# Kernel tuning notes

Hardware: AMD Instinct MI355X
Metric: run time of the kernel (lower is better)

## Reference

```python
import jax, jax.numpy as jnp
import numpy as np

B, N, M, H = 32, 1024, 256, 128


def setup_inputs() -> dict:
    key = jax.random.key(0)
    kA, kh, kW1, kW2 = jax.random.split(key, 4)
    A = jax.random.uniform(kA, (B, N, N), dtype=jnp.float32)
    h = jax.random.normal(kh, (B, N, M), dtype=jnp.float32)
    # torch Linear default init scale ~ 1/sqrt(fan_in)
    W1 = jax.random.normal(kW1, (M, H), dtype=jnp.float32) / np.sqrt(M)
    b1 = jnp.zeros((H,), dtype=jnp.float32)
    W2 = jax.random.normal(kW2, (H, M), dtype=jnp.float32) / np.sqrt(H)
    b2 = jnp.zeros((M,), dtype=jnp.float32)
    return {"A": A, "h": h, "W1": W1, "b1": b1, "W2": W2, "b2": b2}


def reference(A, h, W1, b1, W2, b2):
    # k = bmm(A, h) / 3 : [B,N,M]
    k = jnp.einsum('bij,bjm->bim', A, h) / 3.0
    # eta_g: Linear -> ReLU -> Linear
    k = jax.nn.relu(k @ W1 + b1) @ W2 + b2
    # A_mask = max over last dim of A, keepdims -> [B,N,1]
    A_mask = jnp.max(A, axis=-1, keepdims=True)
    # gated combine: k*mask + h*(mask-1)*(-1) == k*mask + h*(1-mask)
    return k * A_mask + h * (1.0 - A_mask)
```

## Files before the change

kernel.cpp:

```cpp
#include <hip/hip_runtime.h>

typedef __attribute__((ext_vector_type(8))) short bf16x8;
typedef __attribute__((ext_vector_type(4))) float f32x4;
typedef __attribute__((ext_vector_type(8))) unsigned short u16x8;

#define BB 32
#define NN 1024
#define MM 256
#define HH 128

__device__ __forceinline__ unsigned short f2bf(float f) {
  union { float f; unsigned int u; } c; c.f = f;
  unsigned int u = c.u + 0x7fffu + ((c.u >> 16) & 1u);
  return (unsigned short)(u >> 16);
}
__device__ __forceinline__ unsigned int pack2(float lo, float hi) {
  return (unsigned int)f2bf(lo) | ((unsigned int)f2bf(hi) << 16);
}

__global__ __launch_bounds__(256)
void k_transpose_h(const float* __restrict__ hg, unsigned short* __restrict__ hTg) {
  __shared__ unsigned short tile[64][65];
  int bid = blockIdx.x;
  int b = bid >> 6;
  int t = bid & 63;
  int k0 = (t >> 2) << 6;
  int m0 = (t & 3) << 6;
  int tt = threadIdx.x;
  {
    int r = tt >> 2;
    int cg = (tt & 3) << 4;
    const float* src = hg + (((size_t)b * NN + k0 + r) * MM + m0 + cg);
#pragma unroll
    for (int i = 0; i < 4; ++i) {
      float4 v = reinterpret_cast<const float4*>(src)[i];
      tile[r][cg + i * 4 + 0] = f2bf(v.x);
      tile[r][cg + i * 4 + 1] = f2bf(v.y);
      tile[r][cg + i * 4 + 2] = f2bf(v.z);
      tile[r][cg + i * 4 + 3] = f2bf(v.w);
    }
  }
  __syncthreads();
  {
    int mr = tt >> 2;
    int kc = (tt & 3) << 4;
    alignas(16) unsigned short tmp[16];
#pragma unroll
    for (int i = 0; i < 16; ++i) tmp[i] = tile[kc + i][mr];
    unsigned short* dst = hTg + (((size_t)b * MM + m0 + mr) * NN + k0 + kc);
    *reinterpret_cast<u16x8*>(dst)     = *reinterpret_cast<u16x8*>(tmp);
    *reinterpret_cast<u16x8*>(dst + 8) = *reinterpret_cast<u16x8*>(tmp + 8);
  }
}

__global__ __launch_bounds__(256)
void k_transpose_w(const float* __restrict__ W1, const float* __restrict__ W2,
                   unsigned short* __restrict__ W1T, unsigned short* __restrict__ W2T) {
  int idx = blockIdx.x * 256 + threadIdx.x;
  if (idx < MM * HH) {
    int hc = idx >> 8;
    int m  = idx & 255;
    W1T[idx] = f2bf(W1[m * HH + hc]);
  } else {
    int j = idx - MM * HH;
    int m  = j >> 7;
    int hd = j & 127;
    W2T[j] = f2bf(W2[hd * MM + m]);
  }
}

__global__ __launch_bounds__(512, 1)
void k_fused(const float* __restrict__ Ag, const float* __restrict__ hg,
             const unsigned short* __restrict__ hTg,
             const unsigned short* __restrict__ W1Tg,
             const unsigned short* __restrict__ W2Tg,
             const float* __restrict__ b1g, const float* __restrict__ b2g,
             float* __restrict__ outg) {
  __shared__ __align__(16) char smem[131072];
  __shared__ float smax[128];

  const int tid  = threadIdx.x;
  const int lane = tid & 63;
  const int wid  = tid >> 6;
  const int wr   = wid >> 2;
  const int wc   = wid & 3;
  const int l15  = lane & 15;
  const int lg   = lane >> 4;

  const int bid = blockIdx.x;
  const int b   = bid >> 3;
  const int r0  = (bid & 7) << 7;

  const float* Ab = Ag + ((size_t)b * NN + r0) * NN;
  const unsigned short* hTb = hTg + (size_t)b * MM * NN;

  f32x4 acc[4][4];
#pragma unroll
  for (int m = 0; m < 4; ++m)
#pragma unroll
    for (int n = 0; n < 4; ++n) acc[m][n] = f32x4{0.f, 0.f, 0.f, 0.f};

  float pmax = -1e30f;
  const int arow = tid >> 2;
  const int acg  = (tid & 3) << 4;

  for (int k0 = 0; k0 < NN; k0 += 64) {
    {
      const float* src = Ab + (size_t)arow * NN + k0 + acg;
      float4 v0 = reinterpret_cast<const float4*>(src)[0];
      float4 v1 = reinterpret_cast<const float4*>(src)[1];
      float4 v2 = reinterpret_cast<const float4*>(src)[2];
      float4 v3 = reinterpret_cast<const float4*>(src)[3];
      float m0 = fmaxf(fmaxf(v0.x, v0.y), fmaxf(v0.z, v0.w));
      float m1 = fmaxf(fmaxf(v1.x, v1.y), fmaxf(v1.z, v1.w));
      float m2 = fmaxf(fmaxf(v2.x, v2.y), fmaxf(v2.z, v2.w));
      float m3 = fmaxf(fmaxf(v3.x, v3.y), fmaxf(v3.z, v3.w));
      pmax = fmaxf(pmax, fmaxf(fmaxf(m0, m1), fmaxf(m2, m3)));
      unsigned int p0 = pack2(v0.x, v0.y), p1 = pack2(v0.z, v0.w);
      unsigned int p2 = pack2(v1.x, v1.y), p3 = pack2(v1.z, v1.w);
      unsigned int p4 = pack2(v2.x, v2.y), p5 = pack2(v2.z, v2.w);
      unsigned int p6 = pack2(v3.x, v3.y), p7 = pack2(v3.z, v3.w);
      int base = arow * 128;
      int sw   = (arow & 7) << 4;
      *reinterpret_cast<uint4*>(smem + base + ((acg * 2) ^ sw))      = make_uint4(p0, p1, p2, p3);
      *reinterpret_cast<uint4*>(smem + base + ((acg * 2 + 16) ^ sw)) = make_uint4(p4, p5, p6, p7);
    }
    {
      const int hc = (tid & 7) << 3;
#pragma unroll
      for (int i = 0; i < 4; ++i) {
        int hrow = (i << 6) + (tid >> 3);
        uint4 v = *reinterpret_cast<const uint4*>(hTb + (size_t)hrow * NN + k0 + hc);
        *reinterpret_cast<uint4*>(smem + 16384 + hrow * 128 + ((hc * 2) ^ ((hrow & 7) << 4))) = v;
      }
    }
    __syncthreads();
#pragma unroll
    for (int kk = 0; kk < 2; ++kk) {
      const int kb = (kk * 32 + (lg << 3)) * 2;
      bf16x8 af[4], bfr[4];
#pragma unroll
      for (int m = 0; m < 4; ++m) {
        int row = (wr << 6) + (m << 4) + l15;
        af[m] = *reinterpret_cast<const bf16x8*>(smem + row * 128 + (kb ^ ((row & 7) << 4)));
      }
#pragma unroll
      for (int n = 0; n < 4; ++n) {
        int col = (wc << 6) + (n << 4) + l15;
        bfr[n] = *reinterpret_cast<const bf16x8*>(smem + 16384 + col * 128 + (kb ^ ((col & 7) << 4)));
      }
#pragma unroll
      for (int m = 0; m < 4; ++m)
#pragma unroll
        for (int n = 0; n < 4; ++n)
          acc[m][n] = __builtin_amdgcn_mfma_f32_16x16x32_bf16(af[m], bfr[n], acc[m][n], 0, 0, 0);
    }
    __syncthreads();
  }

  {
    float v = pmax;
    v = fmaxf(v, __shfl_xor(v, 1));
    v = fmaxf(v, __shfl_xor(v, 2));
    if ((tid & 3) == 0) smax[arow] = v;
  }

  {
    const float inv3 = 1.0f / 3.0f;
#pragma unroll
    for (int m = 0; m < 4; ++m)
#pragma unroll
      for (int n = 0; n < 4; ++n) {
        int col = (wc << 6) + (n << 4) + l15;
#pragma unroll
        for (int j = 0; j < 4; ++j) {
          int row = (wr << 6) + (m << 4) + (lg << 2) + j;
          *reinterpret_cast<unsigned short*>(smem + row * 512 + ((col * 2) ^ ((row & 7) << 4))) =
              f2bf(acc[m][n][j] * inv3);
        }
      }
  }
  {
#pragma unroll
    for (int i = 0; i < 8; ++i) {
      int c = (i << 9) + tid;
      int row = c >> 5;
      int bc  = (c & 31) << 4;
      uint4 v = *reinterpret_cast<const uint4*>(W1Tg + ((size_t)c << 3));
      *reinterpret_cast<uint4*>(smem + 65536 + row * 512 + (bc ^ ((row & 7) << 4))) = v;
    }
  }
  __syncthreads();

  f32x4 acc1[4][2];
#pragma unroll
  for (int m = 0; m < 4; ++m)
#pragma unroll
    for (int n = 0; n < 2; ++n) acc1[m][n] = f32x4{0.f, 0.f, 0.f, 0.f};
#pragma unroll
  for (int kk = 0; kk < 8; ++kk) {
    const int kb = (kk * 32 + (lg << 3)) * 2;
    bf16x8 af[4], bfr[2];
#pragma unroll
    for (int m = 0; m < 4; ++m) {
      int row = (wr << 6) + (m << 4) + l15;
      af[m] = *reinterpret_cast<const bf16x8*>(smem + row * 512 + (kb ^ ((row & 7) << 4)));
    }
#pragma unroll
    for (int n = 0; n < 2; ++n) {
      int col = (wc << 5) + (n << 4) + l15;
      bfr[n] = *reinterpret_cast<const bf16x8*>(smem + 65536 + col * 512 + (kb ^ ((col & 7) << 4)));
    }
#pragma unroll
    for (int m = 0; m < 4; ++m)
#pragma unroll
      for (int n = 0; n < 2; ++n)
        acc1[m][n] = __builtin_amdgcn_mfma_f32_16x16x32_bf16(af[m], bfr[n], acc1[m][n], 0, 0, 0);
  }
  __syncthreads();

  {
#pragma unroll
    for (int n = 0; n < 2; ++n) {
      int col = (wc << 5) + (n << 4) + l15;
      float bias = b1g[col];
#pragma unroll
      for (int m = 0; m < 4; ++m)
#pragma unroll
        for (int j = 0; j < 4; ++j) {
          int row = (wr << 6) + (m << 4) + (lg << 2) + j;
          float v = fmaxf(acc1[m][n][j] + bias, 0.f);
          *reinterpret_cast<unsigned short*>(smem + row * 256 + ((col * 2) ^ ((row & 7) << 4))) = f2bf(v);
        }
    }
  }
  {
#pragma unroll
    for (int i = 0; i < 8; ++i) {
      int c = (i << 9) + tid;
      int row = c >> 4;
      int bc  = (c & 15) << 4;
      uint4 v = *reinterpret_cast<const uint4*>(W2Tg + ((size_t)c << 3));
      *reinterpret_cast<uint4*>(smem + 65536 + row * 256 + (bc ^ ((row & 7) << 4))) = v;
    }
  }
  __syncthreads();

  f32x4 acc2[4][4];
#pragma unroll
  for (int m = 0; m < 4; ++m)
#pragma unroll
    for (int n = 0; n < 4; ++n) acc2[m][n] = f32x4{0.f, 0.f, 0.f, 0.f};
#pragma unroll
  for (int kk = 0; kk < 4; ++kk) {
    const int kb = (kk * 32 + (lg << 3)) * 2;
    bf16x8 af[4], bfr[4];
#pragma unroll
    for (int m = 0; m < 4; ++m) {
      int row = (wr << 6) + (m << 4) + l15;
      af[m] = *reinterpret_cast<const bf16x8*>(smem + row * 256 + (kb ^ ((row & 7) << 4)));
    }
#pragma unroll
    for (int n = 0; n < 4; ++n) {
      int col = (wc << 6) + (n << 4) + l15;
      bfr[n] = *reinterpret_cast<const bf16x8*>(smem + 65536 + col * 256 + (kb ^ ((col & 7) << 4)));
    }
#pragma unroll
    for (int m = 0; m < 4; ++m)
#pragma unroll
      for (int n = 0; n < 4; ++n)
        acc2[m][n] = __builtin_amdgcn_mfma_f32_16x16x32_bf16(af[m], bfr[n], acc2[m][n], 0, 0, 0);
  }

  {
#pragma unroll
    for (int n = 0; n < 4; ++n) {
      int col = (wc << 6) + (n << 4) + l15;
      float b2v = b2g[col];
#pragma unroll
      for (int m = 0; m < 4; ++m)
#pragma unroll
        for (int j = 0; j < 4; ++j) {
          int row = (wr << 6) + (m << 4) + (lg << 2) + j;
          float kv = acc2[m][n][j] + b2v;
          float mask = smax[row];
          size_t gidx = ((size_t)b * NN + r0 + row) * MM + col;
          float hv = hg[gidx];
          outg[gidx] = kv * mask + hv * (1.f - mask);
        }
    }
  }
}

extern "C" void kernel_launch(void* const* d_in, const int* in_sizes, int n_in,
                              void* d_out, int out_size, void* d_ws, size_t ws_size,
                              hipStream_t stream) {
  (void)in_sizes; (void)n_in; (void)out_size; (void)ws_size;
  const float* A  = (const float*)d_in[0];
  const float* h  = (const float*)d_in[1];
  const float* W1 = (const float*)d_in[2];
  const float* b1 = (const float*)d_in[3];
  const float* W2 = (const float*)d_in[4];
  const float* b2 = (const float*)d_in[5];
  float* out = (float*)d_out;

  unsigned short* hT  = (unsigned short*)d_ws;
  unsigned short* W1T = (unsigned short*)((char*)d_ws + (size_t)BB * MM * NN * 2);
  unsigned short* W2T = W1T + MM * HH;

  k_transpose_h<<<BB * 64, 256, 0, stream>>>(h, hT);
  k_transpose_w<<<256, 256, 0, stream>>>(W1, W2, W1T, W2T);
  k_fused<<<BB * 8, 512, 0, stream>>>(A, h, hT, W1T, W2T, b1, b2, out);
}
```

Measured before the change: 71.80 us.

## Double-buffer A/h tiles in LDS with register prefetch, remap blocks across batches

The main loop becomes a two-stage software pipeline. Global loads for the next 64-wide K slice of A and hT are issued into registers before the current slice is converted and written to one of two LDS buffers. This leaves one barrier per slice instead of two, and global-load latency overlaps with MFMA work. Block indexing is also changed so consecutive blocks cover different batches instead of consecutive row tiles of the same batch. The cost is extra VGPRs for the in-flight prefetch registers and twice the LDS staging space.

```diff
diff --git a/kernel.cpp b/kernel.cpp
--- a/kernel.cpp
+++ b/kernel.cpp
@@ -69,6 +69,48 @@
   }
 }
 
+#define A0_OFF 0
+#define A1_OFF 16384
+#define H0_OFF 32768
+#define H1_OFF 65536
+
+__device__ __forceinline__ void issueA(const float* src, float4 r[4]) {
+#pragma unroll
+  for (int i = 0; i < 4; ++i) r[i] = reinterpret_cast<const float4*>(src)[i];
+}
+__device__ __forceinline__ void issueH(const unsigned short* src, uint4 r[4]) {
+#pragma unroll
+  for (int i = 0; i < 4; ++i) r[i] = *reinterpret_cast<const uint4*>(src + (size_t)i * 64 * NN);
+}
+__device__ __forceinline__ float cvtWriteA(char* smem, int arow, int acg, const float4 r[4]) {
+  float m0 = fmaxf(fmaxf(r[0].x, r[0].y), fmaxf(r[0].z, r[0].w));
+  float m1 = fmaxf(fmaxf(r[1].x, r[1].y), fmaxf(r[1].z, r[1].w));
+  float m2 = fmaxf(fmaxf(r[2].x, r[2].y), fmaxf(r[2].z, r[2].w));
+  float m3 = fmaxf(fmaxf(r[3].x, r[3].y), fmaxf(r[3].z, r[3].w));
+  unsigned int p0 = pack2(r[0].x, r[0].y), p1 = pack2(r[0].z, r[0].w);
+  unsigned int p2 = pack2(r[1].x, r[1].y), p3 = pack2(r[1].z, r[1].w);
+  unsigned int p4 = pack2(r[2].x, r[2].y), p5 = pack2(r[2].z, r[2].w);
+  unsigned int p6 = pack2(r[3].x, r[3].y), p7 = pack2(r[3].z, r[3].w);
+  int base = arow * 128;
+  int sw   = (arow & 7) << 4;
+  *reinterpret_cast<uint4*>(smem + base + ((acg * 2) ^ sw))      = make_uint4(p0, p1, p2, p3);
+  *reinterpret_cast<uint4*>(smem + base + ((acg * 2 + 16) ^ sw)) = make_uint4(p4, p5, p6, p7);
+  return fmaxf(fmaxf(m0, m1), fmaxf(m2, m3));
+}
+__device__ __forceinline__ void writeH(char* smem, int tid, const uint4 r[4]) {
+  const int hc = (tid & 7) << 3;
+#pragma unroll
+  for (int i = 0; i < 4; ++i) {
+    int hrow = (i << 6) + (tid >> 3);
+    *reinterpret_cast<uint4*>(smem + hrow * 128 + ((hc * 2) ^ ((hrow & 7) << 4))) = r[i];
+  }
+}
+
+#define PIPE_BARRIER() do { \
+  asm volatile("s_waitcnt lgkmcnt(0)" ::: "memory"); \
+  __builtin_amdgcn_s_barrier(); \
+  asm volatile("" ::: "memory"); } while (0)
+
 __global__ __launch_bounds__(512, 1)
 void k_fused(const float* __restrict__ Ag, const float* __restrict__ hg,
              const unsigned short* __restrict__ hTg,
@@ -88,8 +130,8 @@
   const int lg   = lane >> 4;
 
   const int bid = blockIdx.x;
-  const int b   = bid >> 3;
-  const int r0  = (bid & 7) << 7;
+  const int b   = bid & 31;
+  const int r0  = (bid >> 5) << 7;
 
   const float* Ab = Ag + ((size_t)b * NN + r0) * NN;
   const unsigned short* hTb = hTg + (size_t)b * MM * NN;
@@ -103,60 +145,59 @@
   float pmax = -1e30f;
   const int arow = tid >> 2;
   const int acg  = (tid & 3) << 4;
-
-  for (int k0 = 0; k0 < NN; k0 += 64) {
-    {
-      const float* src = Ab + (size_t)arow * NN + k0 + acg;
-      float4 v0 = reinterpret_cast<const float4*>(src)[0];
-      float4 v1 = reinterpret_cast<const float4*>(src)[1];
-      float4 v2 = reinterpret_cast<const float4*>(src)[2];
-      float4 v3 = reinterpret_cast<const float4*>(src)[3];
-      float m0 = fmaxf(fmaxf(v0.x, v0.y), fmaxf(v0.z, v0.w));
-      float m1 = fmaxf(fmaxf(v1.x, v1.y), fmaxf(v1.z, v1.w));
-      float m2 = fmaxf(fmaxf(v2.x, v2.y), fmaxf(v2.z, v2.w));
-      float m3 = fmaxf(fmaxf(v3.x, v3.y), fmaxf(v3.z, v3.w));
-      pmax = fmaxf(pmax, fmaxf(fmaxf(m0, m1), fmaxf(m2, m3)));
-      unsigned int p0 = pack2(v0.x, v0.y), p1 = pack2(v0.z, v0.w);
-      unsigned int p2 = pack2(v1.x, v1.y), p3 = pack2(v1.z, v1.w);
-      unsigned int p4 = pack2(v2.x, v2.y), p5 = pack2(v2.z, v2.w);
-      unsigned int p6 = pack2(v3.x, v3.y), p7 = pack2(v3.z, v3.w);
-      int base = arow * 128;
-      int sw   = (arow & 7) << 4;
-      *reinterpret_cast<uint4*>(smem + base + ((acg * 2) ^ sw))      = make_uint4(p0, p1, p2, p3);
-      *reinterpret_cast<uint4*>(smem + base + ((acg * 2 + 16) ^ sw)) = make_uint4(p4, p5, p6, p7);
-    }
-    {
-      const int hc = (tid & 7) << 3;
-#pragma unroll
-      for (int i = 0; i < 4; ++i) {
-        int hrow = (i << 6) + (tid >> 3);
-        uint4 v = *reinterpret_cast<const uint4*>(hTb + (size_t)hrow * NN + k0 + hc);
-        *reinterpret_cast<uint4*>(smem + 16384 + hrow * 128 + ((hc * 2) ^ ((hrow & 7) << 4))) = v;
-      }
-    }
-    __syncthreads();
-#pragma unroll
-    for (int kk = 0; kk < 2; ++kk) {
-      const int kb = (kk * 32 + (lg << 3)) * 2;
-      bf16x8 af[4], bfr[4];
-#pragma unroll
-      for (int m = 0; m < 4; ++m) {
-        int row = (wr << 6) + (m << 4) + l15;
-        af[m] = *reinterpret_cast<const bf16x8*>(smem + row * 128 + (kb ^ ((row & 7) << 4)));
-      }
-#pragma unroll
-      for (int n = 0; n < 4; ++n) {
-        int col = (wc << 6) + (n << 4) + l15;
-        bfr[n] = *reinterpret_cast<const bf16x8*>(smem + 16384 + col * 128 + (kb ^ ((col & 7) << 4)));
-      }
-#pragma unroll
-      for (int m = 0; m < 4; ++m)
-#pragma unroll
-        for (int n = 0; n < 4; ++n)
-          acc[m][n] = __builtin_amdgcn_mfma_f32_16x16x32_bf16(af[m], bfr[n], acc[m][n], 0, 0, 0);
-    }
-    __syncthreads();
-  }
+  const float* Asrc = Ab + (size_t)arow * NN + acg;
+  const unsigned short* Hsrc = hTb + (size_t)(tid >> 3) * NN + ((tid & 7) << 3);
+
+  float4 a0[4], a1[4];
+  uint4  h0[4], h1[4];
+
+#define CONSUME(AOFF, HOFF)                                                          \
+  do {                                                                               \
+    _Pragma("unroll")                                                                \
+    for (int kk = 0; kk < 2; ++kk) {                                                 \
+      const int kb = (kk * 32 + (lg << 3)) * 2;                                      \
+      bf16x8 af[4], bfr[4];                                                          \
+      _Pragma("unroll")                                                              \
+      for (int m = 0; m < 4; ++m) {                                                  \
+        int row = (wr << 6) + (m << 4) + l15;                                        \
+        af[m] = *reinterpret_cast<const bf16x8*>(smem + (AOFF) + row * 128 +         \
+                                                 (kb ^ ((row & 7) << 4)));           \
+      }                                                                              \
+      _Pragma("unroll")                                                              \
+      for (int n = 0; n < 4; ++n) {                                                  \
+        int col = (wc << 6) + (n << 4) + l15;                                        \
+        bfr[n] = *reinterpret_cast<const bf16x8*>(smem + (HOFF) + col * 128 +        \
+                                                  (kb ^ ((col & 7) << 4)));          \
+      }                                                                              \
+      _Pragma("unroll")                                                              \
+      for (int m = 0; m < 4; ++m)                                                    \
+        _Pragma("unroll")                                                            \
+        for (int n = 0; n < 4; ++n)                                                  \
+          acc[m][n] = __builtin_amdgcn_mfma_f32_16x16x32_bf16(af[m], bfr[n],         \
+                                                              acc[m][n], 0, 0, 0);   \
+    }                                                                                \
+  } while (0)
+
+  issueA(Asrc, a0);
+  issueH(Hsrc, h0);
+  for (int t2 = 0; t2 < 8; ++t2) {
+    const int k0 = t2 << 7;
+    issueA(Asrc + k0 + 64, a1);
+    issueH(Hsrc + k0 + 64, h1);
+    pmax = fmaxf(pmax, cvtWriteA(smem + A0_OFF, arow, acg, a0));
+    writeH(smem + H0_OFF, tid, h0);
+    PIPE_BARRIER();
+    CONSUME(A0_OFF, H0_OFF);
+    if (t2 != 7) {
+      issueA(Asrc + k0 + 128, a0);
+      issueH(Hsrc + k0 + 128, h0);
+    }
+    pmax = fmaxf(pmax, cvtWriteA(smem + A1_OFF, arow, acg, a1));
+    writeH(smem + H1_OFF, tid, h1);
+    PIPE_BARRIER();
+    CONSUME(A1_OFF, H1_OFF);
+  }
+  __syncthreads();
 
   {
     float v = pmax;
@@ -290,6 +331,7 @@
         }
     }
   }
+#undef CONSUME
 }
 
 extern "C" void kernel_launch(void* const* d_in, const int* in_sizes, int n_in,
```

After: 75.98 us. 5.8% more time.

## Retile fused kernel to 32-row blocks with register-prefetched A/h pipeline

Applied to the files above, without the earlier changes.

Shrinks each block from 128 rows/512 threads to 32 rows/256 threads, launching 1024 blocks with about 24KB of LDS so several blocks can fit per CU. The A tile is prefetched four stages ahead into registers and double-buffered in LDS, while h fragments are loaded straight from global memory into registers instead of going through LDS. W1/W2 fragments are also read directly from global memory. The aim is to hide global-load latency and raise occupancy on a bandwidth-bound kernel, at the cost of more register pressure and h being re-read by four times as many blocks.

```diff
diff --git a/kernel.cpp b/kernel.cpp
--- a/kernel.cpp
+++ b/kernel.cpp
@@ -69,219 +69,227 @@
   }
 }
 
-__global__ __launch_bounds__(512, 1)
+#define ABUF(i) ((i) * 4096)
+#define KLD 8192
+#define CLD 0
+
+#define PIPE_BARRIER() do { \
+  asm volatile("s_waitcnt lgkmcnt(0)" ::: "memory"); \
+  __builtin_amdgcn_s_barrier(); } while (0)
+
+__global__ __launch_bounds__(256, 3)
 void k_fused(const float* __restrict__ Ag, const float* __restrict__ hg,
              const unsigned short* __restrict__ hTg,
              const unsigned short* __restrict__ W1Tg,
              const unsigned short* __restrict__ W2Tg,
              const float* __restrict__ b1g, const float* __restrict__ b2g,
              float* __restrict__ outg) {
-  __shared__ __align__(16) char smem[131072];
-  __shared__ float smax[128];
+  __shared__ __align__(16) char smem[24576];
+  __shared__ float smax[32];
 
   const int tid  = threadIdx.x;
   const int lane = tid & 63;
   const int wid  = tid >> 6;
-  const int wr   = wid >> 2;
-  const int wc   = wid & 3;
   const int l15  = lane & 15;
   const int lg   = lane >> 4;
+  const int wcol = wid << 6;
 
   const int bid = blockIdx.x;
-  const int b   = bid >> 3;
-  const int r0  = (bid & 7) << 7;
+  const int b   = bid & 31;
+  const int r0  = (bid >> 5) << 5;
 
   const float* Ab = Ag + ((size_t)b * NN + r0) * NN;
   const unsigned short* hTb = hTg + (size_t)b * MM * NN;
 
-  f32x4 acc[4][4];
-#pragma unroll
-  for (int m = 0; m < 4; ++m)
+  f32x4 acc[2][4];
+#pragma unroll
+  for (int m = 0; m < 2; ++m)
 #pragma unroll
     for (int n = 0; n < 4; ++n) acc[m][n] = f32x4{0.f, 0.f, 0.f, 0.f};
 
   float pmax = -1e30f;
-  const int arow = tid >> 2;
-  const int acg  = (tid & 3) << 4;
-
-  for (int k0 = 0; k0 < NN; k0 += 64) {
-    {
-      const float* src = Ab + (size_t)arow * NN + k0 + acg;
-      float4 v0 = reinterpret_cast<const float4*>(src)[0];
-      float4 v1 = reinterpret_cast<const float4*>(src)[1];
-      float4 v2 = reinterpret_cast<const float4*>(src)[2];
-      float4 v3 = reinterpret_cast<const float4*>(src)[3];
-      float m0 = fmaxf(fmaxf(v0.x, v0.y), fmaxf(v0.z, v0.w));
-      float m1 = fmaxf(fmaxf(v1.x, v1.y), fmaxf(v1.z, v1.w));
-      float m2 = fmaxf(fmaxf(v2.x, v2.y), fmaxf(v2.z, v2.w));
-      float m3 = fmaxf(fmaxf(v3.x, v3.y), fmaxf(v3.z, v3.w));
-      pmax = fmaxf(pmax, fmaxf(fmaxf(m0, m1), fmaxf(m2, m3)));
-      unsigned int p0 = pack2(v0.x, v0.y), p1 = pack2(v0.z, v0.w);
-      unsigned int p2 = pack2(v1.x, v1.y), p3 = pack2(v1.z, v1.w);
-      unsigned int p4 = pack2(v2.x, v2.y), p5 = pack2(v2.z, v2.w);
-      unsigned int p6 = pack2(v3.x, v3.y), p7 = pack2(v3.z, v3.w);
-      int base = arow * 128;
-      int sw   = (arow & 7) << 4;
-      *reinterpret_cast<uint4*>(smem + base + ((acg * 2) ^ sw))      = make_uint4(p0, p1, p2, p3);
-      *reinterpret_cast<uint4*>(smem + base + ((acg * 2 + 16) ^ sw)) = make_uint4(p4, p5, p6, p7);
-    }
-    {
-      const int hc = (tid & 7) << 3;
-#pragma unroll
-      for (int i = 0; i < 4; ++i) {
-        int hrow = (i << 6) + (tid >> 3);
-        uint4 v = *reinterpret_cast<const uint4*>(hTb + (size_t)hrow * NN + k0 + hc);
-        *reinterpret_cast<uint4*>(smem + 16384 + hrow * 128 + ((hc * 2) ^ ((hrow & 7) << 4))) = v;
-      }
-    }
-    __syncthreads();
-#pragma unroll
-    for (int kk = 0; kk < 2; ++kk) {
-      const int kb = (kk * 32 + (lg << 3)) * 2;
-      bf16x8 af[4], bfr[4];
-#pragma unroll
-      for (int m = 0; m < 4; ++m) {
-        int row = (wr << 6) + (m << 4) + l15;
-        af[m] = *reinterpret_cast<const bf16x8*>(smem + row * 128 + (kb ^ ((row & 7) << 4)));
-      }
-#pragma unroll
-      for (int n = 0; n < 4; ++n) {
-        int col = (wc << 6) + (n << 4) + l15;
-        bfr[n] = *reinterpret_cast<const bf16x8*>(smem + 16384 + col * 128 + (kb ^ ((col & 7) << 4)));
-      }
-#pragma unroll
-      for (int m = 0; m < 4; ++m)
-#pragma unroll
-        for (int n = 0; n < 4; ++n)
-          acc[m][n] = __builtin_amdgcn_mfma_f32_16x16x32_bf16(af[m], bfr[n], acc[m][n], 0, 0, 0);
-    }
-    __syncthreads();
+  const int arow = tid >> 3;
+  const int acg  = (tid & 7) << 3;
+  const float* Asrc = Ab + (size_t)arow * NN + acg;
+
+  float4  ar[4][2];
+  bf16x8  hb[2][2][4];
+
+#define ISSUEA(R, K0)                                                        \
+  do {                                                                       \
+    (R)[0] = reinterpret_cast<const float4*>(Asrc + (K0))[0];                \
+    (R)[1] = reinterpret_cast<const float4*>(Asrc + (K0))[1];                \
+  } while (0)
+
+#define LOADH(H, K0)                                                         \
+  do {                                                                       \
+    _Pragma("unroll")                                                        \
+    for (int kk = 0; kk < 2; ++kk)                                           \
+      _Pragma("unroll")                                                      \
+      for (int n = 0; n < 4; ++n)                                            \
+        (H)[kk][n] = *reinterpret_cast<const bf16x8*>(                       \
+            hTb + (size_t)(wcol + (n << 4) + l15) * NN + (K0) + kk * 32 +    \
+            (lg << 3));                                                      \
+  } while (0)
+
+#define CVTWRA(BASE, R)                                                      \
+  do {                                                                       \
+    float m0 = fmaxf(fmaxf((R)[0].x, (R)[0].y), fmaxf((R)[0].z, (R)[0].w));  \
+    float m1 = fmaxf(fmaxf((R)[1].x, (R)[1].y), fmaxf((R)[1].z, (R)[1].w));  \
+    pmax = fmaxf(pmax, fmaxf(m0, m1));                                       \
+    unsigned int p0 = pack2((R)[0].x, (R)[0].y), p1 = pack2((R)[0].z, (R)[0].w); \
+    unsigned int p2 = pack2((R)[1].x, (R)[1].y), p3 = pack2((R)[1].z, (R)[1].w); \
+    *reinterpret_cast<uint4*>(smem + (BASE) + arow * 128 +                   \
+                              (((acg << 1)) ^ ((arow & 7) << 4))) =          \
+        make_uint4(p0, p1, p2, p3);                                          \
+  } while (0)
+
+#define CONS(BASE, H)                                                        \
+  do {                                                                       \
+    _Pragma("unroll")                                                        \
+    for (int kk = 0; kk < 2; ++kk) {                                         \
+      bf16x8 af[2];                                                          \
+      _Pragma("unroll")                                                      \
+      for (int m = 0; m < 2; ++m) {                                          \
+        int row = (m << 4) + l15;                                            \
+        af[m] = *reinterpret_cast<const bf16x8*>(                            \
+            smem + (BASE) + row * 128 +                                      \
+            (((kk * 32 + (lg << 3)) * 2) ^ ((row & 7) << 4)));               \
+      }                                                                      \
+      _Pragma("unroll")                                                      \
+      for (int m = 0; m < 2; ++m)                                            \
+        _Pragma("unroll")                                                    \
+        for (int n = 0; n < 4; ++n)                                          \
+          acc[m][n] = __builtin_amdgcn_mfma_f32_16x16x32_bf16(af[m],         \
+              (H)[kk][n], acc[m][n], 0, 0, 0);                               \
+    }                                                                        \
+  } while (0)
+
+#pragma unroll
+  for (int t = 0; t < 4; ++t) ISSUEA(ar[t], t * 64);
+  LOADH(hb[0], 0);
+  LOADH(hb[1], 64);
+  CVTWRA(ABUF(0), ar[0]);
+  PIPE_BARRIER();
+
+#pragma unroll
+  for (int t = 0; t < 16; ++t) {
+    if (t + 4 < 16) ISSUEA(ar[t & 3], (t + 4) * 64);
+    CONS(ABUF(t & 1), hb[t & 1]);
+    if (t + 1 < 16) CVTWRA(ABUF((t + 1) & 1), ar[(t + 1) & 3]);
+    if (t + 2 < 16) LOADH(hb[t & 1], (t + 2) * 64);
+    PIPE_BARRIER();
   }
 
   {
     float v = pmax;
     v = fmaxf(v, __shfl_xor(v, 1));
     v = fmaxf(v, __shfl_xor(v, 2));
-    if ((tid & 3) == 0) smax[arow] = v;
+    v = fmaxf(v, __shfl_xor(v, 4));
+    if ((tid & 7) == 0) smax[arow] = v;
   }
 
   {
     const float inv3 = 1.0f / 3.0f;
 #pragma unroll
-    for (int m = 0; m < 4; ++m)
+    for (int m = 0; m < 2; ++m)
 #pragma unroll
       for (int n = 0; n < 4; ++n) {
-        int col = (wc << 6) + (n << 4) + l15;
+        int col = wcol + (n << 4) + l15;
 #pragma unroll
         for (int j = 0; j < 4; ++j) {
-          int row = (wr << 6) + (m << 4) + (lg << 2) + j;
-          *reinterpret_cast<unsigned short*>(smem + row * 512 + ((col * 2) ^ ((row & 7) << 4))) =
+          int row = (m << 4) + (lg << 2) + j;
+          *reinterpret_cast<unsigned short*>(smem + KLD + row * 512 +
+                                             ((col * 2) ^ ((row & 7) << 4))) =
               f2bf(acc[m][n][j] * inv3);
         }
       }
   }
-  {
-#pragma unroll
-    for (int i = 0; i < 8; ++i) {
-      int c = (i << 9) + tid;
-      int row = c >> 5;
-      int bc  = (c & 31) << 4;
-      uint4 v = *reinterpret_cast<const uint4*>(W1Tg + ((size_t)c << 3));
-      *reinterpret_cast<uint4*>(smem + 65536 + row * 512 + (bc ^ ((row & 7) << 4))) = v;
-    }
-  }
-  __syncthreads();
-
-  f32x4 acc1[4][2];
-#pragma unroll
-  for (int m = 0; m < 4; ++m)
+  PIPE_BARRIER();
+
+  f32x4 acc1[2][2];
+#pragma unroll
+  for (int m = 0; m < 2; ++m)
 #pragma unroll
     for (int n = 0; n < 2; ++n) acc1[m][n] = f32x4{0.f, 0.f, 0.f, 0.f};
-#pragma unroll
-  for (int kk = 0; kk < 8; ++kk) {
-    const int kb = (kk * 32 + (lg << 3)) * 2;
-    bf16x8 af[4], bfr[2];
-#pragma unroll
-    for (int m = 0; m < 4; ++m) {
-      int row = (wr << 6) + (m << 4) + l15;
-      af[m] = *reinterpret_cast<const bf16x8*>(smem + row * 512 + (kb ^ ((row & 7) << 4)));
+  const int wcol1 = wid << 5;
+#pragma unroll
+  for (int kq = 0; kq < 8; ++kq) {
+    bf16x8 af[2], bw[2];
+#pragma unroll
+    for (int m = 0; m < 2; ++m) {
+      int row = (m << 4) + l15;
+      af[m] = *reinterpret_cast<const bf16x8*>(smem + KLD + row * 512 +
+              (((kq * 32 + (lg << 3)) * 2) ^ ((row & 7) << 4)));
     }
 #pragma unroll
     for (int n = 0; n < 2; ++n) {
-      int col = (wc << 5) + (n << 4) + l15;
-      bfr[n] = *reinterpret_cast<const bf16x8*>(smem + 65536 + col * 512 + (kb ^ ((col & 7) << 4)));
-    }
-#pragma unroll
-    for (int m = 0; m < 4; ++m)
+      int col = wcol1 + (n << 4) + l15;
+      bw[n] = *reinterpret_cast<const bf16x8*>(W1Tg + (size_t)col * 256 +
+                                               kq * 32 + (lg << 3));
+    }
+#pragma unroll
+    for (int m = 0; m < 2; ++m)
 #pragma unroll
       for (int n = 0; n < 2; ++n)
-        acc1[m][n] = __builtin_amdgcn_mfma_f32_16x16x32_bf16(af[m], bfr[n], acc1[m][n], 0, 0, 0);
-  }
-  __syncthreads();
+        acc1[m][n] = __builtin_amdgcn_mfma_f32_16x16x32_bf16(af[m], bw[n], acc1[m][n], 0, 0, 0);
+  }
 
   {
 #pragma unroll
     for (int n = 0; n < 2; ++n) {
-      int col = (wc << 5) + (n << 4) + l15;
+      int col = wcol1 + (n << 4) + l15;
       float bias = b1g[col];
 #pragma unroll
-      for (int m = 0; m < 4; ++m)
+      for (int m = 0; m < 2; ++m)
 #pragma unroll
         for (int j = 0; j < 4; ++j) {
-          int row = (wr << 6) + (m << 4) + (lg << 2) + j;
+          int row = (m << 4) + (lg << 2) + j;
           float v = fmaxf(acc1[m][n][j] + bias, 0.f);
-          *reinterpret_cast<unsigned short*>(smem + row * 256 + ((col * 2) ^ ((row & 7) << 4))) = f2bf(v);
+          *reinterpret_cast<unsigned short*>(smem + CLD + row * 256 +
+                                             ((col * 2) ^ ((row & 7) << 4))) = f2bf(v);
         }
     }
   }
-  {
-#pragma unroll
-    for (int i = 0; i < 8; ++i) {
-      int c = (i << 9) + tid;
-      int row = c >> 4;
-      int bc  = (c & 15) << 4;
-      uint4 v = *reinterpret_cast<const uint4*>(W2Tg + ((size_t)c << 3));
-      *reinterpret_cast<uint4*>(smem + 65536 + row * 256 + (bc ^ ((row & 7) << 4))) = v;
-    }
-  }
-  __syncthreads();
-
-  f32x4 acc2[4][4];
-#pragma unroll
-  for (int m = 0; m < 4; ++m)
+  PIPE_BARRIER();
+
+  f32x4 acc2[2][4];
+#pragma unroll
+  for (int m = 0; m < 2; ++m)
 #pragma unroll
     for (int n = 0; n < 4; ++n) acc2[m][n] = f32x4{0.f, 0.f, 0.f, 0.f};
 #pragma unroll
-  for (int kk = 0; kk < 4; ++kk) {
-    const int kb = (kk * 32 + (lg << 3)) * 2;
-    bf16x8 af[4], bfr[4];
-#pragma unroll
-    for (int m = 0; m < 4; ++m) {
-      int row = (wr << 6) + (m << 4) + l15;
-      af[m] = *reinterpret_cast<const bf16x8*>(smem + row * 256 + (kb ^ ((row & 7) << 4)));
+  for (int kq = 0; kq < 4; ++kq) {
+    bf16x8 af[2], bw[4];
+#pragma unroll
+    for (int m = 0; m < 2; ++m) {
+      int row = (m << 4) + l15;
+      af[m] = *reinterpret_cast<const bf16x8*>(smem + CLD + row * 256 +
+              (((kq * 32 + (lg << 3)) * 2) ^ ((row & 7) << 4)));
     }
 #pragma unroll
     for (int n = 0; n < 4; ++n) {
-      int col = (wc << 6) + (n << 4) + l15;
-      bfr[n] = *reinterpret_cast<const bf16x8*>(smem + 65536 + col * 256 + (kb ^ ((col & 7) << 4)));
-    }
-#pragma unroll
-    for (int m = 0; m < 4; ++m)
+      int col = wcol + (n << 4) + l15;
+      bw[n] = *reinterpret_cast<const bf16x8*>(W2Tg + (size_t)col * 128 +
+                                               kq * 32 + (lg << 3));
+    }
+#pragma unroll
+    for (int m = 0; m < 2; ++m)
 #pragma unroll
       for (int n = 0; n < 4; ++n)
-        acc2[m][n] = __builtin_amdgcn_mfma_f32_16x16x32_bf16(af[m], bfr[n], acc2[m][n], 0, 0, 0);
+        acc2[m][n] = __builtin_amdgcn_mfma_f32_16x16x32_bf16(af[m], bw[n], acc2[m][n], 0, 0, 0);
   }
 
   {
 #pragma unroll
     for (int n = 0; n < 4; ++n) {
-      int col = (wc << 6) + (n << 4) + l15;
+      int col = wcol + (n << 4) + l15;
       float b2v = b2g[col];
 #pragma unroll
-      for (int m = 0; m < 4; ++m)
+      for (int m = 0; m < 2; ++m)
 #pragma unroll
         for (int j = 0; j < 4; ++j) {
-          int row = (wr << 6) + (m << 4) + (lg << 2) + j;
+          int row = (m << 4) + (lg << 2) + j;
           float kv = acc2[m][n][j] + b2v;
           float mask = smax[row];
           size_t gidx = ((size_t)b * NN + r0 + row) * MM + col;
@@ -290,6 +298,10 @@
         }
     }
   }
+#undef CONS
+#undef CVTWRA
+#undef LOADH
+#undef ISSUEA
 }
 
 extern "C" void kernel_launch(void* const* d_in, const int* in_sizes, int n_in,
@@ -310,5 +322,5 @@
 
   k_transpose_h<<<BB * 64, 256, 0, stream>>>(h, hT);
   k_transpose_w<<<256, 256, 0, stream>>>(W1, W2, W1T, W2T);
-  k_fused<<<BB * 8, 512, 0, stream>>>(A, h, hT, W1T, W2T, b1, b2, out);
-}
+  k_fused<<<BB * 32, 256, 0, stream>>>(A, h, hT, W1T, W2T, b1, b2, out);
+}
```

Result: slower. 99.11 us (+38.0%).

## Double-buffer main GEMM with direct global-to-LDS loads and read weights from global

Applied to the files above, without the earlier changes.

The main A·h loop now streams fp32 A and bf16 hT tiles straight into LDS with global_load_lds, double-buffered so the next tile's load overlaps the current tile's MFMAs. The fp32-to-bf16 conversion and the row max move to the consumer side, after the LDS read. Block-to-batch mapping is interleaved (b = bid & 31) to change how blocks spread across the device. The MLP stages now read W1T/W2T fragments directly from global/L2 instead of staging them through LDS, which removes some barriers. The cost is twice the LDS traffic for fp32 A, conversion work repeated across the four column waves, and uncoalesced weight reads.

```diff
diff --git a/kernel.cpp b/kernel.cpp
--- a/kernel.cpp
+++ b/kernel.cpp
@@ -16,6 +16,12 @@
 }
 __device__ __forceinline__ unsigned int pack2(float lo, float hi) {
   return (unsigned int)f2bf(lo) | ((unsigned int)f2bf(hi) << 16);
+}
+
+typedef __attribute__((address_space(3))) unsigned int as3_u32;
+typedef const __attribute__((address_space(1))) unsigned int as1_u32;
+__device__ __forceinline__ void gl_lds16(const void* g, void* l) {
+  __builtin_amdgcn_global_load_lds((as1_u32*)g, (as3_u32*)l, 16, 0, 0);
 }
 
 __global__ __launch_bounds__(256)
@@ -69,6 +75,15 @@
   }
 }
 
+#define ABUF(x) ((x) * 32768)
+#define HBUF(x) (65536 + (x) * 32768)
+#define KLD 0
+#define CLD 65536
+
+#define PIPE_BARRIER() do { \
+  asm volatile("s_waitcnt lgkmcnt(0)" ::: "memory"); \
+  __builtin_amdgcn_s_barrier(); } while (0)
+
 __global__ __launch_bounds__(512, 1)
 void k_fused(const float* __restrict__ Ag, const float* __restrict__ hg,
              const unsigned short* __restrict__ hTg,
@@ -88,141 +103,151 @@
   const int lg   = lane >> 4;
 
   const int bid = blockIdx.x;
-  const int b   = bid >> 3;
-  const int r0  = (bid & 7) << 7;
+  const int b   = bid & 31;
+  const int r0  = (bid >> 5) << 7;
 
   const float* Ab = Ag + ((size_t)b * NN + r0) * NN;
   const unsigned short* hTb = hTg + (size_t)b * MM * NN;
 
+  const float* baseA[4];
+  const unsigned short* baseH[4];
+#pragma unroll
+  for (int i = 0; i < 4; ++i) {
+    int c = i * 512 + tid;
+    int row = c >> 4, cic = c & 15;
+    baseA[i] = Ab + (size_t)row * NN + ((cic ^ ((row & 7) << 1)) << 2);
+  }
+#pragma unroll
+  for (int i = 0; i < 4; ++i) {
+    int c = i * 512 + tid;
+    int col = c >> 3, cic = c & 7;
+    baseH[i] = hTb + (size_t)col * NN + ((cic ^ (col & 7)) << 3);
+  }
+  const int ldsW = wid << 10;
+
+#define STAGE(K0, AB, HB)                                                   \
+  do {                                                                      \
+    _Pragma("unroll")                                                       \
+    for (int i = 0; i < 4; ++i)                                             \
+      gl_lds16(baseA[i] + (K0), smem + (AB) + ldsW + i * 8192);             \
+    _Pragma("unroll")                                                       \
+    for (int i = 0; i < 4; ++i)                                             \
+      gl_lds16(baseH[i] + (K0), smem + (HB) + ldsW + i * 8192);             \
+  } while (0)
+
   f32x4 acc[4][4];
 #pragma unroll
   for (int m = 0; m < 4; ++m)
 #pragma unroll
     for (int n = 0; n < 4; ++n) acc[m][n] = f32x4{0.f, 0.f, 0.f, 0.f};
-
-  float pmax = -1e30f;
-  const int arow = tid >> 2;
-  const int acg  = (tid & 3) << 4;
-
-  for (int k0 = 0; k0 < NN; k0 += 64) {
-    {
-      const float* src = Ab + (size_t)arow * NN + k0 + acg;
-      float4 v0 = reinterpret_cast<const float4*>(src)[0];
-      float4 v1 = reinterpret_cast<const float4*>(src)[1];
-      float4 v2 = reinterpret_cast<const float4*>(src)[2];
-      float4 v3 = reinterpret_cast<const float4*>(src)[3];
-      float m0 = fmaxf(fmaxf(v0.x, v0.y), fmaxf(v0.z, v0.w));
-      float m1 = fmaxf(fmaxf(v1.x, v1.y), fmaxf(v1.z, v1.w));
-      float m2 = fmaxf(fmaxf(v2.x, v2.y), fmaxf(v2.z, v2.w));
-      float m3 = fmaxf(fmaxf(v3.x, v3.y), fmaxf(v3.z, v3.w));
-      pmax = fmaxf(pmax, fmaxf(fmaxf(m0, m1), fmaxf(m2, m3)));
-      unsigned int p0 = pack2(v0.x, v0.y), p1 = pack2(v0.z, v0.w);
-      unsigned int p2 = pack2(v1.x, v1.y), p3 = pack2(v1.z, v1.w);
-      unsigned int p4 = pack2(v2.x, v2.y), p5 = pack2(v2.z, v2.w);
-      unsigned int p6 = pack2(v3.x, v3.y), p7 = pack2(v3.z, v3.w);
-      int base = arow * 128;
-      int sw   = (arow & 7) << 4;
-      *reinterpret_cast<uint4*>(smem + base + ((acg * 2) ^ sw))      = make_uint4(p0, p1, p2, p3);
-      *reinterpret_cast<uint4*>(smem + base + ((acg * 2 + 16) ^ sw)) = make_uint4(p4, p5, p6, p7);
-    }
-    {
-      const int hc = (tid & 7) << 3;
-#pragma unroll
-      for (int i = 0; i < 4; ++i) {
-        int hrow = (i << 6) + (tid >> 3);
-        uint4 v = *reinterpret_cast<const uint4*>(hTb + (size_t)hrow * NN + k0 + hc);
-        *reinterpret_cast<uint4*>(smem + 16384 + hrow * 128 + ((hc * 2) ^ ((hrow & 7) << 4))) = v;
-      }
-    }
-    __syncthreads();
-#pragma unroll
-    for (int kk = 0; kk < 2; ++kk) {
-      const int kb = (kk * 32 + (lg << 3)) * 2;
-      bf16x8 af[4], bfr[4];
-#pragma unroll
-      for (int m = 0; m < 4; ++m) {
-        int row = (wr << 6) + (m << 4) + l15;
-        af[m] = *reinterpret_cast<const bf16x8*>(smem + row * 128 + (kb ^ ((row & 7) << 4)));
-      }
+  float pm[4] = {-1e30f, -1e30f, -1e30f, -1e30f};
+
+#define CONSUME(AB, HB)                                                     \
+  do {                                                                      \
+    _Pragma("unroll")                                                       \
+    for (int kk = 0; kk < 2; ++kk) {                                        \
+      bf16x8 af[4], bh[4];                                                  \
+      _Pragma("unroll")                                                     \
+      for (int m = 0; m < 4; ++m) {                                         \
+        int row = (wr << 6) + (m << 4) + l15;                               \
+        int boff = (AB) + row * 256 +                                       \
+                   (((kk << 7) + (lg << 5)) ^ ((row & 7) << 5));            \
+        float4 lo = *reinterpret_cast<const float4*>(smem + boff);          \
+        float4 hi = *reinterpret_cast<const float4*>(smem + boff + 16);     \
+        pm[m] = fmaxf(pm[m],                                                \
+            fmaxf(fmaxf(fmaxf(lo.x, lo.y), fmaxf(lo.z, lo.w)),              \
+                  fmaxf(fmaxf(hi.x, hi.y), fmaxf(hi.z, hi.w))));            \
+        uint4 q = make_uint4(pack2(lo.x, lo.y), pack2(lo.z, lo.w),          \
+                             pack2(hi.x, hi.y), pack2(hi.z, hi.w));         \
+        af[m] = *reinterpret_cast<bf16x8*>(&q);                             \
+      }                                                                     \
+      _Pragma("unroll")                                                     \
+      for (int n = 0; n < 4; ++n) {                                         \
+        int col = (wc << 6) + (n << 4) + l15;                               \
+        bh[n] = *reinterpret_cast<const bf16x8*>(smem + (HB) + col * 128 +  \
+                 (((kk << 6) + (lg << 4)) ^ ((col & 7) << 4)));             \
+      }                                                                     \
+      _Pragma("unroll")                                                     \
+      for (int m = 0; m < 4; ++m)                                           \
+        _Pragma("unroll")                                                   \
+        for (int n = 0; n < 4; ++n)                                         \
+          acc[m][n] = __builtin_amdgcn_mfma_f32_16x16x32_bf16(af[m], bh[n], \
+                                                              acc[m][n], 0, 0, 0); \
+    }                                                                       \
+  } while (0)
+
+  STAGE(0, ABUF(0), HBUF(0));
+
+#pragma unroll
+  for (int t = 0; t < 16; ++t) {
+    __builtin_amdgcn_s_barrier();
+    if (t < 15) STAGE((t + 1) * 64, ABUF((t + 1) & 1), HBUF((t + 1) & 1));
+    if (t < 15) asm volatile("s_waitcnt vmcnt(8)" ::: "memory");
+    else        asm volatile("s_waitcnt vmcnt(0)" ::: "memory");
+    __builtin_amdgcn_s_barrier();
+    if ((t & 1) == 0) CONSUME(ABUF(0), HBUF(0));
+    else              CONSUME(ABUF(1), HBUF(1));
+  }
+
+#pragma unroll
+  for (int m = 0; m < 4; ++m) {
+    float v = pm[m];
+    v = fmaxf(v, __shfl_xor(v, 16));
+    v = fmaxf(v, __shfl_xor(v, 32));
+    if (wc == 0 && lg == 0) smax[(wr << 6) + (m << 4) + l15] = v;
+  }
+  PIPE_BARRIER();
+
+  {
+    const float inv3 = 1.0f / 3.0f;
+#pragma unroll
+    for (int m = 0; m < 4; ++m)
 #pragma unroll
       for (int n = 0; n < 4; ++n) {
         int col = (wc << 6) + (n << 4) + l15;
-        bfr[n] = *reinterpret_cast<const bf16x8*>(smem + 16384 + col * 128 + (kb ^ ((col & 7) << 4)));
-      }
-#pragma unroll
-      for (int m = 0; m < 4; ++m)
-#pragma unroll
-        for (int n = 0; n < 4; ++n)
-          acc[m][n] = __builtin_amdgcn_mfma_f32_16x16x32_bf16(af[m], bfr[n], acc[m][n], 0, 0, 0);
-    }
-    __syncthreads();
-  }
-
-  {
-    float v = pmax;
-    v = fmaxf(v, __shfl_xor(v, 1));
-    v = fmaxf(v, __shfl_xor(v, 2));
-    if ((tid & 3) == 0) smax[arow] = v;
-  }
-
-  {
-    const float inv3 = 1.0f / 3.0f;
-#pragma unroll
-    for (int m = 0; m < 4; ++m)
-#pragma unroll
-      for (int n = 0; n < 4; ++n) {
-        int col = (wc << 6) + (n << 4) + l15;
 #pragma unroll
         for (int j = 0; j < 4; ++j) {
           int row = (wr << 6) + (m << 4) + (lg << 2) + j;
-          *reinterpret_cast<unsigned short*>(smem + row * 512 + ((col * 2) ^ ((row & 7) << 4))) =
+          *reinterpret_cast<unsigned short*>(smem + KLD + row * 512 +
+                                             ((col * 2) ^ ((row & 7) << 4))) =
               f2bf(acc[m][n][j] * inv3);
         }
       }
   }
-  {
-#pragma unroll
-    for (int i = 0; i < 8; ++i) {
-      int c = (i << 9) + tid;
-      int row = c >> 5;
-      int bc  = (c & 31) << 4;
-      uint4 v = *reinterpret_cast<const uint4*>(W1Tg + ((size_t)c << 3));
-      *reinterpret_cast<uint4*>(smem + 65536 + row * 512 + (bc ^ ((row & 7) << 4))) = v;
-    }
-  }
-  __syncthreads();
+  PIPE_BARRIER();
 
   f32x4 acc1[4][2];
 #pragma unroll
   for (int m = 0; m < 4; ++m)
 #pragma unroll
     for (int n = 0; n < 2; ++n) acc1[m][n] = f32x4{0.f, 0.f, 0.f, 0.f};
-#pragma unroll
-  for (int kk = 0; kk < 8; ++kk) {
-    const int kb = (kk * 32 + (lg << 3)) * 2;
-    bf16x8 af[4], bfr[2];
+  const int wcol1 = wc << 5;
+#pragma unroll
+  for (int kq = 0; kq < 8; ++kq) {
+    bf16x8 af[4], bw[2];
 #pragma unroll
     for (int m = 0; m < 4; ++m) {
       int row = (wr << 6) + (m << 4) + l15;
-      af[m] = *reinterpret_cast<const bf16x8*>(smem + row * 512 + (kb ^ ((row & 7) << 4)));
+      af[m] = *reinterpret_cast<const bf16x8*>(smem + KLD + row * 512 +
+              (((kq * 32 + (lg << 3)) * 2) ^ ((row & 7) << 4)));
     }
 #pragma unroll
     for (int n = 0; n < 2; ++n) {
-      int col = (wc << 5) + (n << 4) + l15;
-      bfr[n] = *reinterpret_cast<const bf16x8*>(smem + 65536 + col * 512 + (kb ^ ((col & 7) << 4)));
+      int col = wcol1 + (n << 4) + l15;
+      bw[n] = *reinterpret_cast<const bf16x8*>(W1Tg + (size_t)col * 256 +
+                                               kq * 32 + (lg << 3));
     }
 #pragma unroll
     for (int m = 0; m < 4; ++m)
 #pragma unroll
       for (int n = 0; n < 2; ++n)
-        acc1[m][n] = __builtin_amdgcn_mfma_f32_16x16x32_bf16(af[m], bfr[n], acc1[m][n], 0, 0, 0);
-  }
-  __syncthreads();
+        acc1[m][n] = __builtin_amdgcn_mfma_f32_16x16x32_bf16(af[m], bw[n], acc1[m][n], 0, 0, 0);
+  }
 
   {
 #pragma unroll
     for (int n = 0; n < 2; ++n) {
-      int col = (wc << 5) + (n << 4) + l15;
+      int col = wcol1 + (n << 4) + l15;
       float bias = b1g[col];
 #pragma unroll
       for (int m = 0; m < 4; ++m)
@@ -230,21 +255,12 @@
         for (int j = 0; j < 4; ++j) {
           int row = (wr << 6) + (m << 4) + (lg << 2) + j;
           float v = fmaxf(acc1[m][n][j] + bias, 0.f);
-          *reinterpret_cast<unsigned short*>(smem + row * 256 + ((col * 2) ^ ((row & 7) << 4))) = f2bf(v);
+          *reinterpret_cast<unsigned short*>(smem + CLD + row * 256 +
+                                             ((col * 2) ^ ((row & 7) << 4))) = f2bf(v);
         }
     }
   }
-  {
-#pragma unroll
-    for (int i = 0; i < 8; ++i) {
-      int c = (i << 9) + tid;
-      int row = c >> 4;
-      int bc  = (c & 15) << 4;
-      uint4 v = *reinterpret_cast<const uint4*>(W2Tg + ((size_t)c << 3));
-      *reinterpret_cast<uint4*>(smem + 65536 + row * 256 + (bc ^ ((row & 7) << 4))) = v;
-    }
-  }
-  __syncthreads();
+  PIPE_BARRIER();
 
   f32x4 acc2[4][4];
 #pragma unroll
@@ -252,24 +268,25 @@
 #pragma unroll
     for (int n = 0; n < 4; ++n) acc2[m][n] = f32x4{0.f, 0.f, 0.f, 0.f};
 #pragma unroll
-  for (int kk = 0; kk < 4; ++kk) {
-    const int kb = (kk * 32 + (lg << 3)) * 2;
-    bf16x8 af[4], bfr[4];
+  for (int kq = 0; kq < 4; ++kq) {
+    bf16x8 af[4], bw[4];
 #pragma unroll
     for (int m = 0; m < 4; ++m) {
       int row = (wr << 6) + (m << 4) + l15;
-      af[m] = *reinterpret_cast<const bf16x8*>(smem + row * 256 + (kb ^ ((row & 7) << 4)));
+      af[m] = *reinterpret_cast<const bf16x8*>(smem + CLD + row * 256 +
+              (((kq * 32 + (lg << 3)) * 2) ^ ((row & 7) << 4)));
     }
 #pragma unroll
     for (int n = 0; n < 4; ++n) {
       int col = (wc << 6) + (n << 4) + l15;
-      bfr[n] = *reinterpret_cast<const bf16x8*>(smem + 65536 + col * 256 + (kb ^ ((col & 7) << 4)));
+      bw[n] = *reinterpret_cast<const bf16x8*>(W2Tg + (size_t)col * 128 +
+                                               kq * 32 + (lg << 3));
     }
 #pragma unroll
     for (int m = 0; m < 4; ++m)
 #pragma unroll
       for (int n = 0; n < 4; ++n)
-        acc2[m][n] = __builtin_amdgcn_mfma_f32_16x16x32_bf16(af[m], bfr[n], acc2[m][n], 0, 0, 0);
+        acc2[m][n] = __builtin_amdgcn_mfma_f32_16x16x32_bf16(af[m], bw[n], acc2[m][n], 0, 0, 0);
   }
 
   {
@@ -290,6 +307,8 @@
         }
     }
   }
+#undef CONSUME
+#undef STAGE
 }
 
 extern "C" void kernel_launch(void* const* d_in, const int* in_sizes, int n_in,
```

After: 76.44 us. +6.5%, slower.
